# Performance work log

Measured on AMD Instinct MI355X. Metric: run time of the kernel, lower is better.

Reference implementation:

```python
import jax, jax.numpy as jnp
import numpy as np

N, E, G = 40000, 640000, 64
D, H, O = 128, 128, 10
EPS = 1e-5


def _lin(k, fan_in, shape):
    b = 1.0 / np.sqrt(fan_in)
    return jax.random.uniform(k, shape, jnp.float32, -b, b)


def setup_inputs() -> dict:
    key = jax.random.key(0)
    ks = jax.random.split(key, 12)
    x = jax.random.normal(ks[0], (N, D), jnp.float32)
    edge_index = jax.random.randint(ks[1], (2, E), 0, N)
    batch = jnp.sort(jax.random.randint(ks[2], (N,), 0, G))
    return {
        "x": x,
        "edge_index": edge_index,
        "batch": batch,
        "num_graphs": G,
        "W_gcn": _lin(ks[3], D, (D, H)),
        "b_gcn": jnp.zeros((H,), jnp.float32),
        "gamma": jnp.ones((H,), jnp.float32),
        "beta": jnp.zeros((H,), jnp.float32),
        "W1": _lin(ks[4], 3 * H, (3 * H, H)),
        "b1": _lin(ks[5], 3 * H, (H,)),
        "W2": _lin(ks[6], H, (H, H // 2)),
        "b2": _lin(ks[7], H, (H // 2,)),
        "W3": _lin(ks[8], H // 2, (H // 2, O)),
        "b3": _lin(ks[9], H // 2, (O,)),
    }


def reference(x, edge_index, batch, num_graphs, W_gcn, b_gcn, gamma, beta, W1, b1, W2, b2, W3, b3):
    n = x.shape[0]
    src, dst = edge_index[0], edge_index[1]
    # GCNConv: h = D^{-1/2} (A + I) D^{-1/2} (x W) + b  (self-loops, symmetric norm)
    h = x @ W_gcn                                   # [N, H]
    deg = jax.ops.segment_sum(jnp.ones((src.shape[0],), h.dtype), dst, num_segments=n) + 1.0
    dinv = jax.lax.rsqrt(deg)                       # [N]
    coef = dinv[src] * dinv[dst]                    # [E]
    msg = h[src] * coef[:, None]                    # [E, H] gather (memory bound)
    agg = jax.ops.segment_sum(msg, dst, num_segments=n)
    agg = agg + h * (dinv * dinv)[:, None] + b_gcn  # self-loop term + bias
    h = jax.nn.relu(agg)
    # LayerNorm over feature dim
    mu = jnp.mean(h, axis=-1, keepdims=True)
    var = jnp.mean(jnp.square(h - mu), axis=-1, keepdims=True)
    h = (h - mu) * jax.lax.rsqrt(var + EPS) * gamma + beta
    # global mean / add / max pools keyed by graph id
    counts = jax.ops.segment_sum(jnp.ones((n,), h.dtype), batch, num_segments=num_graphs)
    x_add = jax.ops.segment_sum(h, batch, num_segments=num_graphs)
    x_mean = x_add / jnp.maximum(counts, 1.0)[:, None]
    x_max = jax.ops.segment_max(h, batch, num_segments=num_graphs)
    x_max = jnp.where(counts[:, None] > 0, x_max, 0.0)
    g = jnp.concatenate([x_mean, x_add, x_max], axis=1)  # [G, 3H]
    # MLP head (dropout is identity at inference)
    g = jax.nn.relu(g @ W1 + b1)
    g = jax.nn.relu(g @ W2 + b2)
    return g @ W3 + b3
```

## Files before the change

kernel.cpp:

```cpp
#include <hip/hip_runtime.h>
#include <math.h>

#define EPS 1e-5f
#define FLT_BIG 3.402823466e38f

typedef __attribute__((ext_vector_type(8))) short bf16x8;
typedef __attribute__((ext_vector_type(4))) float f32x4;

__device__ __forceinline__ unsigned fflip(float f){
  int i = __float_as_int(f);
  return (unsigned)(i ^ ((i>>31) | 0x80000000));
}
__device__ __forceinline__ float funflip(unsigned u){
  int i = (u & 0x80000000u) ? (int)(u ^ 0x80000000u) : (int)(~u);
  return __int_as_float(i);
}
__device__ __forceinline__ unsigned f2bf(float f){
  unsigned u = __float_as_uint(f);
  return (u + 0x7FFFu + ((u>>16)&1u)) >> 16;
}
__device__ __forceinline__ float bf_lo(unsigned v){ return __uint_as_float(v<<16); }
__device__ __forceinline__ float bf_hi(unsigned v){ return __uint_as_float(v & 0xFFFF0000u); }

__device__ __forceinline__ int lbound(const int* __restrict__ a, int n, int key){
  int lo=0, hi=n;
  while(lo<hi){ int mid=(lo+hi)>>1; if(a[mid]<key) lo=mid+1; else hi=mid; }
  return lo;
}

__global__ __launch_bounds__(256) void k_init(
    unsigned* __restrict__ psum, unsigned* __restrict__ pmaxu, int GP,
    const float* __restrict__ Wg, ushort* __restrict__ Wp,
    const int* __restrict__ batch, int N, int* __restrict__ gcnt, int G,
    unsigned* __restrict__ gcur, int NB){
  int i = blockIdx.x*blockDim.x + threadIdx.x;
  if(i<GP){ psum[i]=0u; pmaxu[i]=0u; }
  if(i<NB) gcur[i]=0u;
  if(i<G){
    int s = lbound(batch,N,i), e = lbound(batch,N,i+1);
    gcnt[i] = e - s;
  }
  if(i<2048){
    int tile = i>>6, l = i&63;
    int kt = tile>>3, ct = tile&7;
    int q = l>>4, nn = l&15;
    ushort w8[8];
    #pragma unroll
    for(int j=0;j<8;j++)
      w8[j] = (ushort)f2bf(Wg[(kt*32 + q*8 + j)*128 + ct*16 + nn]);
    ushort* dst = Wp + (size_t)i*8;
    #pragma unroll
    for(int j=0;j<8;j++) dst[j] = w8[j];
  }
}

__global__ __launch_bounds__(256) void k_bucketize(
    const int* __restrict__ src, const int* __restrict__ dst, int E, int NB,
    unsigned* __restrict__ gcur, unsigned* __restrict__ dstream){
  __shared__ unsigned hist[160];
  __shared__ unsigned excl[160];
  __shared__ unsigned base[160];
  __shared__ unsigned wsum[4];
  __shared__ unsigned lsorted[2048];
  int t = threadIdx.x, bid = blockIdx.x;
  int e0 = bid*2048 + t*8;
  unsigned rec[8]; int bk[8]; unsigned rr[8];
  #pragma unroll
  for(int j=0;j<8;j++) bk[j] = -1;
  if(e0+7 < E){
    int4 s0 = *(const int4*)(src+e0), s1 = *(const int4*)(src+e0+4);
    int4 d0 = *(const int4*)(dst+e0), d1 = *(const int4*)(dst+e0+4);
    int ss[8] = {s0.x,s0.y,s0.z,s0.w,s1.x,s1.y,s1.z,s1.w};
    int dd[8] = {d0.x,d0.y,d0.z,d0.w,d1.x,d1.y,d1.z,d1.w};
    #pragma unroll
    for(int j=0;j<8;j++){
      bk[j] = dd[j]>>8;
      rec[j] = ((unsigned)bk[j]<<24) | ((unsigned)(dd[j]&255)<<16) | (unsigned)ss[j];
    }
  } else {
    #pragma unroll
    for(int j=0;j<8;j++){
      int ee = e0+j;
      if(ee<E){
        int s = src[ee], d = dst[ee];
        bk[j] = d>>8;
        rec[j] = ((unsigned)bk[j]<<24) | ((unsigned)(d&255)<<16) | (unsigned)s;
      }
    }
  }
  for(int i=t;i<NB;i+=256) hist[i]=0u;
  __syncthreads();
  #pragma unroll
  for(int j=0;j<8;j++)
    if(bk[j]>=0) rr[j] = atomicAdd(&hist[bk[j]],1u);
  __syncthreads();
  unsigned hv = (t<NB)?hist[t]:0u;
  unsigned v = hv;
  int lane = t & 63;
  #pragma unroll
  for(int d=1; d<64; d<<=1){
    unsigned o = __shfl_up(v, d, 64);
    if(lane >= d) v += o;
  }
  if(lane==63) wsum[t>>6] = v;
  __syncthreads();
  {
    unsigned pre = 0;
    int w = t>>6;
    if(w>0) pre += wsum[0];
    if(w>1) pre += wsum[1];
    if(w>2) pre += wsum[2];
    if(t<NB) excl[t] = v + pre - hv;
  }
  if(t<NB){
    int ridx = t + bid; while(ridx>=NB) ridx-=NB;
    base[ridx] = atomicAdd(&gcur[ridx], hist[ridx]);
  }
  __syncthreads();
  #pragma unroll
  for(int j=0;j<8;j++)
    if(bk[j]>=0) lsorted[excl[bk[j]]+rr[j]] = rec[j];
  __syncthreads();
  int vc = E - bid*2048; if(vc>2048) vc=2048;
  #pragma unroll
  for(int j=0;j<8;j++){
    int k = j*256 + t;
    if(k<vc){
      unsigned rc = lsorted[k];
      unsigned bb = rc>>24;
      unsigned pos = base[bb] + (unsigned)k - excl[bb];
      if(pos < 8192u) dstream[((size_t)bb<<13) + pos] = rc;
    }
  }
}

__global__ __launch_bounds__(1024) void k_csrscale(
    const unsigned* __restrict__ dstream, const unsigned* __restrict__ gcur,
    int N, ushort* __restrict__ csr, int* __restrict__ cursor,
    const float4* __restrict__ x4, uint2* __restrict__ xs2){
  __shared__ unsigned cnt[256];
  __shared__ float dv[256];
  __shared__ ushort slab[16384];
  int b = blockIdx.x, t = threadIdx.x;
  if(t<256) cnt[t]=0u;
  __syncthreads();
  int nb = (int)gcur[b]; if(nb>8192) nb=8192;
  const unsigned* sp = dstream + ((size_t)b<<13);
  for(int i=t;i<nb;i+=1024){
    unsigned rc = sp[i];
    int dl = (rc>>16)&255;
    unsigned p = atomicAdd(&cnt[dl],1u);
    if(p<64u) slab[(dl<<6)+(int)p] = (ushort)(rc & 0xFFFFu);
  }
  __syncthreads();
  const uint4* s4 = (const uint4*)slab;
  uint4* c4 = ((uint4*)csr) + ((size_t)b<<11);
  #pragma unroll
  for(int i=t;i<2048;i+=1024) c4[i] = s4[i];
  if(t<256){
    int node = (b<<8) + t;
    if(node<N) cursor[node] = (int)cnt[t];
    int deg = (int)cnt[t]; if(deg>64) deg=64;
    dv[t] = rsqrtf((float)deg + 1.0f);
  }
  __syncthreads();
  int base = b<<8;
  for(int i=t; i<8192; i+=1024){
    int nl = i>>5;
    int node = base + nl;
    if(node<N){
      float dinv = dv[nl];
      size_t idx = ((size_t)node<<5) + (i&31);
      float4 v = x4[idx];
      uint2 o;
      o.x = (f2bf(v.y*dinv)<<16) | f2bf(v.x*dinv);
      o.y = (f2bf(v.w*dinv)<<16) | f2bf(v.z*dinv);
      xs2[idx] = o;
    }
  }
}

__global__ void k_agg(const uint4* __restrict__ xs4, const int* __restrict__ cursor,
                      const ushort* __restrict__ csr, int n, uint4* __restrict__ zb4){
  int w = (blockIdx.x*blockDim.x + threadIdx.x)>>6;
  if(w>=n) return;
  int lane = threadIdx.x & 63;
  int grp = lane>>4, li = lane&15;
  int deg = cursor[w]; if(deg>64) deg=64;
  int k0 = w<<6, k1 = k0+deg;
  float dd = rsqrtf((float)deg + 1.0f);
  float a0=0.f,a1=0.f,a2=0.f,a3=0.f,a4=0.f,a5=0.f,a6=0.f,a7=0.f;
  if(grp==0){
    uint4 sv = xs4[(w<<4)+li];
    a0=bf_lo(sv.x); a1=bf_hi(sv.x); a2=bf_lo(sv.y); a3=bf_hi(sv.y);
    a4=bf_lo(sv.z); a5=bf_hi(sv.z); a6=bf_lo(sv.w); a7=bf_hi(sv.w);
  }
  for(int kb=k0; kb<k1; kb+=16){
    int base = kb + (grp<<2);
    ushort4 s4 = *(const ushort4*)(csr + base);
    if(base   < k1){ uint4 v = xs4[((int)s4.x<<4)+li];
      a0+=bf_lo(v.x); a1+=bf_hi(v.x); a2+=bf_lo(v.y); a3+=bf_hi(v.y);
      a4+=bf_lo(v.z); a5+=bf_hi(v.z); a6+=bf_lo(v.w); a7+=bf_hi(v.w); }
    if(base+1 < k1){ uint4 v = xs4[((int)s4.y<<4)+li];
      a0+=bf_lo(v.x); a1+=bf_hi(v.x); a2+=bf_lo(v.y); a3+=bf_hi(v.y);
      a4+=bf_lo(v.z); a5+=bf_hi(v.z); a6+=bf_lo(v.w); a7+=bf_hi(v.w); }
    if(base+2 < k1){ uint4 v = xs4[((int)s4.z<<4)+li];
      a0+=bf_lo(v.x); a1+=bf_hi(v.x); a2+=bf_lo(v.y); a3+=bf_hi(v.y);
      a4+=bf_lo(v.z); a5+=bf_hi(v.z); a6+=bf_lo(v.w); a7+=bf_hi(v.w); }
    if(base+3 < k1){ uint4 v = xs4[((int)s4.w<<4)+li];
      a0+=bf_lo(v.x); a1+=bf_hi(v.x); a2+=bf_lo(v.y); a3+=bf_hi(v.y);
      a4+=bf_lo(v.z); a5+=bf_hi(v.z); a6+=bf_lo(v.w); a7+=bf_hi(v.w); }
  }
  a0 += __shfl_xor(a0,16,64); a1 += __shfl_xor(a1,16,64);
  a2 += __shfl_xor(a2,16,64); a3 += __shfl_xor(a3,16,64);
  a4 += __shfl_xor(a4,16,64); a5 += __shfl_xor(a5,16,64);
  a6 += __shfl_xor(a6,16,64); a7 += __shfl_xor(a7,16,64);
  a0 += __shfl_xor(a0,32,64); a1 += __shfl_xor(a1,32,64);
  a2 += __shfl_xor(a2,32,64); a3 += __shfl_xor(a3,32,64);
  a4 += __shfl_xor(a4,32,64); a5 += __shfl_xor(a5,32,64);
  a6 += __shfl_xor(a6,32,64); a7 += __shfl_xor(a7,32,64);
  if(grp==0){
    uint4 o;
    o.x = (f2bf(a1*dd)<<16) | f2bf(a0*dd);
    o.y = (f2bf(a3*dd)<<16) | f2bf(a2*dd);
    o.z = (f2bf(a5*dd)<<16) | f2bf(a4*dd);
    o.w = (f2bf(a7*dd)<<16) | f2bf(a6*dd);
    zb4[(w<<4)+li] = o;
  }
}

__global__ __launch_bounds__(256) void k_gemmln(
    const unsigned* __restrict__ zb, const ushort* __restrict__ Wp,
    const float* __restrict__ bgc, const float* __restrict__ gamma, const float* __restrict__ beta,
    const int* __restrict__ batch, int n,
    float* __restrict__ pool_sum, unsigned* __restrict__ pool_maxu){
  __shared__ unsigned ztu[64*68];
  int t = threadIdx.x, lane = t & 63, wv = t >> 6;
  int rowBase = blockIdx.x*64;
  {
    int row = t>>2, qo = (t&3)*16;
    unsigned* lp = ztu + row*68 + qo;
    if(rowBase+row < n){
      const uint4* gp = (const uint4*)(zb + (size_t)(rowBase+row)*64 + qo);
      #pragma unroll
      for(int i=0;i<4;i++) ((uint4*)lp)[i] = gp[i];
    }else{
      #pragma unroll
      for(int i=0;i<4;i++) ((uint4*)lp)[i] = make_uint4(0,0,0,0);
    }
  }
  __syncthreads();

  int q = lane>>4, nn = lane&15;
  int m = wv*16 + nn;
  bf16x8 afr[4];
  #pragma unroll
  for(int kt=0;kt<4;kt++)
    afr[kt] = *(const bf16x8*)((const char*)ztu + m*272 + kt*64 + q*16);

  f32x4 acc[8];
  #pragma unroll
  for(int ct=0;ct<8;ct++){
    f32x4 c = {0.f,0.f,0.f,0.f};
    #pragma unroll
    for(int kt=0;kt<4;kt++){
      bf16x8 bfr = *(const bf16x8*)(Wp + ((size_t)(kt*8+ct)*64 + lane)*8);
      c = __builtin_amdgcn_mfma_f32_16x16x32_bf16(afr[kt], bfr, c, 0, 0, 0);
    }
    acc[ct] = c;
  }
  float s[4]={0,0,0,0}, qq[4]={0,0,0,0};
  #pragma unroll
  for(int ct=0;ct<8;ct++){
    float bb = bgc[ct*16+nn];
    #pragma unroll
    for(int r=0;r<4;r++){
      float v = acc[ct][r] + bb;
      v = fmaxf(v, 0.f);
      acc[ct][r] = v;
      s[r] += v; qq[r] += v*v;
    }
  }
  #pragma unroll
  for(int d=1; d<16; d<<=1){
    #pragma unroll
    for(int r=0;r<4;r++){
      s[r]  += __shfl_xor(s[r],  d, 64);
      qq[r] += __shfl_xor(qq[r], d, 64);
    }
  }
  float mu[4], isd[4];
  #pragma unroll
  for(int r=0;r<4;r++){
    mu[r] = s[r]*(1.f/128.f);
    float var = qq[r]*(1.f/128.f) - mu[r]*mu[r];
    isd[r] = rsqrtf(var + EPS);
  }
  #pragma unroll
  for(int ct=0;ct<8;ct++){
    float gm = gamma[ct*16+nn], bt = beta[ct*16+nn];
    #pragma unroll
    for(int r=0;r<4;r++)
      acc[ct][r] = (acc[ct][r]-mu[r])*isd[r]*gm + bt;
  }
  int gbr[4];
  #pragma unroll
  for(int r=0;r<4;r++){
    int gr = rowBase + wv*16 + q*4 + r;
    gbr[r] = (gr < n) ? batch[gr] : -1;
  }
  int b0i = rowBase + wv*16; if(b0i >= n) b0i = n-1;
  int b15i = rowBase + wv*16 + 15; if(b15i >= n) b15i = n-1;
  int gmin = batch[b0i], gmax = batch[b15i];
  if(gmax < gmin) gmax = gmin;
  for(int g=gmin; g<=gmax; ++g){
    #pragma unroll
    for(int ct=0;ct<8;ct++){
      float ssum = 0.f, smax = -FLT_BIG;
      #pragma unroll
      for(int r=0;r<4;r++){
        if(gbr[r]==g){
          ssum += acc[ct][r];
          smax = fmaxf(smax, acc[ct][r]);
        }
      }
      ssum += __shfl_xor(ssum, 16, 64);
      ssum += __shfl_xor(ssum, 32, 64);
      float o1 = __shfl_xor(smax, 16, 64); smax = fmaxf(smax, o1);
      float o2 = __shfl_xor(smax, 32, 64); smax = fmaxf(smax, o2);
      if(q==0){
        if(ssum != 0.f)     atomicAdd(&pool_sum[g*128 + ct*16 + nn], ssum);
        if(smax > -FLT_BIG) atomicMax(&pool_maxu[g*128 + ct*16 + nn], fflip(smax));
      }
    }
  }
}

__global__ __launch_bounds__(512) void k_head(
    const float* __restrict__ pool_sum, const unsigned* __restrict__ pool_maxu,
    const int* __restrict__ gcnt,
    const float* __restrict__ W1, const float* __restrict__ b1,
    const float* __restrict__ W2, const float* __restrict__ b2,
    const float* __restrict__ W3, const float* __restrict__ b3,
    float* __restrict__ out){
  int g = blockIdx.x, t = threadIdx.x;
  __shared__ float red[4][128];
  __shared__ float gl[384];
  __shared__ float h1[128];
  __shared__ float h2[64];
  int cnt = gcnt[g];
  if(t<384){
    int j = t & 127;
    if(t<128){
      gl[t] = pool_sum[g*128+j] / (float)((cnt>1)?cnt:1);
    } else if(t<256){
      gl[t] = pool_sum[g*128+j];
    } else {
      float m = funflip(pool_maxu[g*128+j]);
      gl[t] = (cnt>0) ? m : 0.f;
    }
  }
  __syncthreads();
  int j = t & 127, kh = t >> 7;
  float p=0.f;
  for(int k=kh*96; k<kh*96+96; k++) p += gl[k]*W1[k*128+j];
  red[kh][j]=p;
  __syncthreads();
  if(t<128){
    float v = red[0][t]+red[1][t]+red[2][t]+red[3][t]+b1[t];
    h1[t]=fmaxf(v,0.f);
  }
  __syncthreads();
  if(t<64){
    float a=b2[t];
    for(int k=0;k<128;k++) a += h1[k]*W2[k*64+t];
    h2[t]=fmaxf(a,0.f);
  }
  __syncthreads();
  if(t<10){
    float a=b3[t];
    for(int k=0;k<64;k++) a += h2[k]*W3[k*10+t];
    out[g*10+t]=a;
  }
}

extern "C" void kernel_launch(void* const* d_in, const int* in_sizes, int n_in,
                              void* d_out, int out_size, void* d_ws, size_t ws_size,
                              hipStream_t stream){
  const float* x     = (const float*)d_in[0];
  const int*   ei    = (const int*)d_in[1];
  const int*   batch = (const int*)d_in[2];
  const float* Wg    = (const float*)d_in[4];
  const float* bg    = (const float*)d_in[5];
  const float* gamma = (const float*)d_in[6];
  const float* beta  = (const float*)d_in[7];
  const float* W1    = (const float*)d_in[8];
  const float* b1    = (const float*)d_in[9];
  const float* W2    = (const float*)d_in[10];
  const float* b2    = (const float*)d_in[11];
  const float* W3    = (const float*)d_in[12];
  const float* b3    = (const float*)d_in[13];
  float* out = (float*)d_out;

  int N = in_sizes[0]/128;
  int E = in_sizes[1]/2;
  const int G = 64;
  const int* src = ei;
  const int* dst = ei + E;
  int NB = (N+255)>>8;

  char* p = (char*)d_ws;
  auto alloc=[&](size_t bytes)->char*{ char* r=p; p += (bytes+255)&~(size_t)255; return r; };
  int*      cursor  = (int*)     alloc((size_t)N*4);
  ushort*   csr     = (ushort*)  alloc((size_t)NB*16384*2);
  unsigned* zb      = (unsigned*)alloc((size_t)N*64*4);
  float*    psum    = (float*)   alloc((size_t)G*128*4);
  unsigned* pmaxu   = (unsigned*)alloc((size_t)G*128*4);
  unsigned* xs      = (unsigned*)alloc((size_t)N*64*4);
  ushort*   Wp      = (ushort*)  alloc(2048*8*2);
  int*      gcnt    = (int*)     alloc((size_t)G*4);
  unsigned* gcur    = (unsigned*)alloc((size_t)NB*4);
  unsigned* dstream = (unsigned*)alloc((size_t)NB*8192*4);

  int GP = G*128;
  k_init<<<32,256,0,stream>>>((unsigned*)psum,pmaxu,GP,Wg,Wp,batch,N,gcnt,G,gcur,NB);
  int bb = (E+2047)/2048;
  k_bucketize<<<bb,256,0,stream>>>(src,dst,E,NB,gcur,dstream);
  k_csrscale<<<NB,1024,0,stream>>>(dstream,gcur,N,csr,cursor,(const float4*)x,(uint2*)xs);
  int ab = (int)(((size_t)N*64 + 255)/256);
  k_agg<<<ab,256,0,stream>>>((const uint4*)xs,cursor,csr,N,(uint4*)zb);
  k_gemmln<<<(N+63)/64,256,0,stream>>>(zb,Wp,bg,gamma,beta,batch,N,psum,pmaxu);
  k_head<<<G,512,0,stream>>>(psum,pmaxu,gcnt,W1,b1,W2,b2,W3,b3,out);
}
```

Before: 164.4 us.

## Remove init kernel: memset zero buffers, fold weight packing into bucketize

New measurement: 162.7 us. About the same (-1.1%).

```diff
diff --git a/kernel.cpp b/kernel.cpp
--- a/kernel.cpp
+++ b/kernel.cpp
@@ -28,41 +28,37 @@
   return lo;
 }
 
-__global__ __launch_bounds__(256) void k_init(
-    unsigned* __restrict__ psum, unsigned* __restrict__ pmaxu, int GP,
-    const float* __restrict__ Wg, ushort* __restrict__ Wp,
-    const int* __restrict__ batch, int N, int* __restrict__ gcnt, int G,
-    unsigned* __restrict__ gcur, int NB){
-  int i = blockIdx.x*blockDim.x + threadIdx.x;
-  if(i<GP){ psum[i]=0u; pmaxu[i]=0u; }
-  if(i<NB) gcur[i]=0u;
-  if(i<G){
-    int s = lbound(batch,N,i), e = lbound(batch,N,i+1);
-    gcnt[i] = e - s;
-  }
-  if(i<2048){
-    int tile = i>>6, l = i&63;
-    int kt = tile>>3, ct = tile&7;
-    int q = l>>4, nn = l&15;
-    ushort w8[8];
-    #pragma unroll
-    for(int j=0;j<8;j++)
-      w8[j] = (ushort)f2bf(Wg[(kt*32 + q*8 + j)*128 + ct*16 + nn]);
-    ushort* dst = Wp + (size_t)i*8;
-    #pragma unroll
-    for(int j=0;j<8;j++) dst[j] = w8[j];
-  }
-}
-
 __global__ __launch_bounds__(256) void k_bucketize(
     const int* __restrict__ src, const int* __restrict__ dst, int E, int NB,
-    unsigned* __restrict__ gcur, unsigned* __restrict__ dstream){
+    unsigned* __restrict__ gcur, unsigned* __restrict__ dstream,
+    const float* __restrict__ Wg, ushort* __restrict__ Wp,
+    const int* __restrict__ batch, int N, int* __restrict__ gcnt, int G){
   __shared__ unsigned hist[160];
   __shared__ unsigned excl[160];
   __shared__ unsigned base[160];
   __shared__ unsigned wsum[4];
   __shared__ unsigned lsorted[2048];
   int t = threadIdx.x, bid = blockIdx.x;
+
+  if(bid < 8){
+    int i = bid*256 + t;
+    int tile = i>>6, l = i&63;
+    int kt = tile>>3, ct = tile&7;
+    int q = l>>4, nn = l&15;
+    ushort w8[8];
+    #pragma unroll
+    for(int j=0;j<8;j++)
+      w8[j] = (ushort)f2bf(Wg[(kt*32 + q*8 + j)*128 + ct*16 + nn]);
+    ushort* dstp = Wp + (size_t)i*8;
+    #pragma unroll
+    for(int j=0;j<8;j++) dstp[j] = w8[j];
+  } else if(bid == 8){
+    if(t < G){
+      int s = lbound(batch,N,t), e = lbound(batch,N,t+1);
+      gcnt[t] = e - s;
+    }
+  }
+
   int e0 = bid*2048 + t*8;
   unsigned rec[8]; int bk[8]; unsigned rr[8];
   #pragma unroll
@@ -234,29 +230,20 @@
     const float* __restrict__ bgc, const float* __restrict__ gamma, const float* __restrict__ beta,
     const int* __restrict__ batch, int n,
     float* __restrict__ pool_sum, unsigned* __restrict__ pool_maxu){
-  __shared__ unsigned ztu[64*68];
   int t = threadIdx.x, lane = t & 63, wv = t >> 6;
   int rowBase = blockIdx.x*64;
-  {
-    int row = t>>2, qo = (t&3)*16;
-    unsigned* lp = ztu + row*68 + qo;
-    if(rowBase+row < n){
-      const uint4* gp = (const uint4*)(zb + (size_t)(rowBase+row)*64 + qo);
-      #pragma unroll
-      for(int i=0;i<4;i++) ((uint4*)lp)[i] = gp[i];
-    }else{
-      #pragma unroll
-      for(int i=0;i<4;i++) ((uint4*)lp)[i] = make_uint4(0,0,0,0);
-    }
-  }
-  __syncthreads();
-
   int q = lane>>4, nn = lane&15;
-  int m = wv*16 + nn;
+  int m = rowBase + wv*16 + nn;
   bf16x8 afr[4];
-  #pragma unroll
-  for(int kt=0;kt<4;kt++)
-    afr[kt] = *(const bf16x8*)((const char*)ztu + m*272 + kt*64 + q*16);
+  if(m < n){
+    const char* rp = (const char*)zb + (size_t)m*256;
+    #pragma unroll
+    for(int kt=0;kt<4;kt++)
+      afr[kt] = *(const bf16x8*)(rp + kt*64 + q*16);
+  } else {
+    #pragma unroll
+    for(int kt=0;kt<4;kt++) afr[kt] = (bf16x8){0,0,0,0,0,0,0,0};
+  }
 
   f32x4 acc[8];
   #pragma unroll
@@ -411,21 +398,22 @@
 
   char* p = (char*)d_ws;
   auto alloc=[&](size_t bytes)->char*{ char* r=p; p += (bytes+255)&~(size_t)255; return r; };
+  size_t zr_bytes = (size_t)G*128*4 + (size_t)G*128*4 + 1024;
+  char*     zr      = alloc(zr_bytes);
+  float*    psum    = (float*)zr;
+  unsigned* pmaxu   = (unsigned*)(zr + (size_t)G*128*4);
+  unsigned* gcur    = (unsigned*)(zr + (size_t)G*128*4*2);
   int*      cursor  = (int*)     alloc((size_t)N*4);
   ushort*   csr     = (ushort*)  alloc((size_t)NB*16384*2);
   unsigned* zb      = (unsigned*)alloc((size_t)N*64*4);
-  float*    psum    = (float*)   alloc((size_t)G*128*4);
-  unsigned* pmaxu   = (unsigned*)alloc((size_t)G*128*4);
   unsigned* xs      = (unsigned*)alloc((size_t)N*64*4);
   ushort*   Wp      = (ushort*)  alloc(2048*8*2);
   int*      gcnt    = (int*)     alloc((size_t)G*4);
-  unsigned* gcur    = (unsigned*)alloc((size_t)NB*4);
   unsigned* dstream = (unsigned*)alloc((size_t)NB*8192*4);
 
-  int GP = G*128;
-  k_init<<<32,256,0,stream>>>((unsigned*)psum,pmaxu,GP,Wg,Wp,batch,N,gcnt,G,gcur,NB);
+  hipMemsetAsync(zr, 0, zr_bytes, stream);
   int bb = (E+2047)/2048;
-  k_bucketize<<<bb,256,0,stream>>>(src,dst,E,NB,gcur,dstream);
+  k_bucketize<<<bb,256,0,stream>>>(src,dst,E,NB,gcur,dstream,Wg,Wp,batch,N,gcnt,G);
   k_csrscale<<<NB,1024,0,stream>>>(dstream,gcur,N,csr,cursor,(const float4*)x,(uint2*)xs);
   int ab = (int)(((size_t)N*64 + 255)/256);
   k_agg<<<ab,256,0,stream>>>((const uint4*)xs,cursor,csr,N,(uint4*)zb);
```
